# Kernel tuning notes

Measured on AMD Instinct MI355X. Metric: run time of the kernel, lower is better.

## Reference

```python
import jax, jax.numpy as jnp
import numpy as np

D_MODEL = 1024
N_HEADS = 16
D_K = D_MODEL // N_HEADS
D_HIDDEN = 2048
LN_EPS = 1e-5


def setup_inputs() -> dict:
    key = jax.random.key(0)
    ks = jax.random.split(key, 16)
    s = 0.02
    inp = {
        'x': jax.random.normal(ks[0], (4, 2048, D_MODEL), dtype=jnp.float32),
        'Wq': jax.random.normal(ks[1], (D_MODEL, D_MODEL), dtype=jnp.float32) * s,
        'bq': jnp.zeros((D_MODEL,), jnp.float32),
        'Wk': jax.random.normal(ks[2], (D_MODEL, D_MODEL), dtype=jnp.float32) * s,
        'bk': jnp.zeros((D_MODEL,), jnp.float32),
        'Wv': jax.random.normal(ks[3], (D_MODEL, D_MODEL), dtype=jnp.float32) * s,
        'bv': jnp.zeros((D_MODEL,), jnp.float32),
        'Wo': jax.random.normal(ks[4], (D_MODEL, D_MODEL), dtype=jnp.float32) * s,
        'bo': jnp.zeros((D_MODEL,), jnp.float32),
        'ln1_g': jnp.ones((D_MODEL,), jnp.float32),
        'ln1_b': jnp.zeros((D_MODEL,), jnp.float32),
        'ln2_g': jnp.ones((D_MODEL,), jnp.float32),
        'ln2_b': jnp.zeros((D_MODEL,), jnp.float32),
        'W1': jax.random.normal(ks[5], (2 * D_HIDDEN, D_MODEL), dtype=jnp.float32) * s,
        'b1': jnp.zeros((2 * D_HIDDEN,), jnp.float32),
        'W2': jax.random.normal(ks[6], (D_MODEL, D_HIDDEN), dtype=jnp.float32) * s,
        'b2': jnp.zeros((D_MODEL,), jnp.float32),
    }
    return inp


def _layernorm(x, g, b):
    mu = jnp.mean(x, axis=-1, keepdims=True)
    var = jnp.mean(jnp.square(x - mu), axis=-1, keepdims=True)
    return (x - mu) * jax.lax.rsqrt(var + LN_EPS) * g + b


def _attention(xn, Wq, bq, Wk, bk, Wv, bv, Wo, bo):
    B, S, _ = xn.shape
    def split_heads(t):  # [B,S,D] -> [B,H,S,Dk]
        return t.reshape(B, S, N_HEADS, D_K).transpose(0, 2, 1, 3)
    Q = split_heads(xn @ Wq.T + bq)
    K = split_heads(xn @ Wk.T + bk)
    V = split_heads(xn @ Wv.T + bv)
    scores = jnp.einsum('bhqd,bhkd->bhqk', Q, K) / jnp.float32(D_K ** 0.5)
    attn = jax.nn.softmax(scores, axis=-1)  # torch code does max-sub + softmax (same math)
    ctx = jnp.einsum('bhqk,bhkd->bhqd', attn, V)
    ctx = ctx.transpose(0, 2, 1, 3).reshape(B, S, D_MODEL)
    return ctx @ Wo.T + bo


def reference(x, Wq, bq, Wk, bk, Wv, bv, Wo, bo, ln1_g, ln1_b, ln2_g, ln2_b, W1, b1, W2, b2):
    # pre-norm attention block
    xn = _layernorm(x, ln1_g, ln1_b)
    x = x + _attention(xn, Wq, bq, Wk, bk, Wv, bv, Wo, bo)
    # pre-norm ReGLU FFN
    xn = _layernorm(x, ln2_g, ln2_b)
    h = xn @ W1.T + b1
    a, b_ = jnp.split(h, 2, axis=-1)
    h = jax.nn.relu(a) * b_
    x = x + (h @ W2.T + b2)
    return x
```

## Files before the change

kernel.cpp:

```cpp
#include <hip/hip_runtime.h>
#include <hip/hip_bf16.h>

typedef __attribute__((ext_vector_type(8))) short short8;
typedef __attribute__((ext_vector_type(4))) float floatx4;

#define LN_EPS 1e-5f
#define EXP2_SCALE 0.18033688011112042f

__device__ __forceinline__ float b2f(unsigned short u) {
    union { float f; unsigned int i; } x; x.i = ((unsigned int)u) << 16; return x.f;
}
__device__ __forceinline__ unsigned short f2b(float f) {
    union { float f; unsigned int i; } x; x.f = f;
    unsigned int r = x.i + 0x7fffu + ((x.i >> 16) & 1u);
    return (unsigned short)(r >> 16);
}
__device__ __forceinline__ float to_f(unsigned short u) { return b2f(u); }
__device__ __forceinline__ float to_f(float f) { return f; }
__device__ __forceinline__ unsigned int cvtpk(float a, float b) {
    unsigned int r;
    asm("v_cvt_pk_bf16_f32 %0, %1, %2" : "=v"(r) : "v"(a), "v"(b));
    return r;
}

__device__ __forceinline__ void async16(const unsigned short* g, unsigned short* l) {
    __builtin_amdgcn_global_load_lds(
        (const __attribute__((address_space(1))) unsigned int*)g,
        (__attribute__((address_space(3))) unsigned int*)l, 16, 0, 0);
}

template<typename T>
__device__ __forceinline__ void ln_row(const T* __restrict__ xr, const float* __restrict__ g,
                                       const float* __restrict__ bb, unsigned short* __restrict__ outr,
                                       float* red)
{
    const int tid = threadIdx.x;
    float v[4];
#pragma unroll
    for (int i = 0; i < 4; i++) v[i] = to_f(xr[tid + i * 256]);
    float s  = v[0] + v[1] + v[2] + v[3];
    float sq = v[0]*v[0] + v[1]*v[1] + v[2]*v[2] + v[3]*v[3];
#pragma unroll
    for (int o = 32; o >= 1; o >>= 1) {
        s  += __shfl_xor(s,  o, 64);
        sq += __shfl_xor(sq, o, 64);
    }
    const int wave = tid >> 6, lane = tid & 63;
    if (lane == 0) { red[wave] = s; red[4 + wave] = sq; }
    __syncthreads();
    s  = red[0] + red[1] + red[2] + red[3];
    sq = red[4] + red[5] + red[6] + red[7];
    const float mu  = s * (1.0f / 1024.0f);
    const float var = sq * (1.0f / 1024.0f) - mu * mu;
    const float rs  = rsqrtf(var + LN_EPS);
#pragma unroll
    for (int i = 0; i < 4; i++) {
        int c = tid + i * 256;
        outr[c] = f2b((v[i] - mu) * rs * g[c] + bb[c]);
    }
}

__global__ __launch_bounds__(256)
void prep_kernel(const float* __restrict__ Wq, const float* __restrict__ Wk,
                 const float* __restrict__ Wv, const float* __restrict__ Wo,
                 const float* __restrict__ W1, const float* __restrict__ W2,
                 unsigned short* __restrict__ wdst,
                 const float* __restrict__ x, const float* __restrict__ ln1g,
                 const float* __restrict__ ln1b, unsigned short* __restrict__ xn)
{
    __shared__ float red[8];
    if (blockIdx.x < 5120) {
        const size_t i = (size_t)(blockIdx.x * 256 + threadIdx.x) * 8;
        const float* src; size_t off;
        if (i < 4194304) {
            int w = (int)(i >> 20);
            src = (w == 0) ? Wq : (w == 1) ? Wk : (w == 2) ? Wv : Wo;
            off = i & 1048575;
        } else if (i < 8388608) { src = W1; off = i - 4194304; }
        else                    { src = W2; off = i - 8388608; }
        float4 a = *reinterpret_cast<const float4*>(src + off);
        float4 b = *reinterpret_cast<const float4*>(src + off + 4);
        short8 r;
        r[0] = (short)f2b(a.x); r[1] = (short)f2b(a.y);
        r[2] = (short)f2b(a.z); r[3] = (short)f2b(a.w);
        r[4] = (short)f2b(b.x); r[5] = (short)f2b(b.y);
        r[6] = (short)f2b(b.z); r[7] = (short)f2b(b.w);
        *reinterpret_cast<short8*>(wdst + i) = r;
    } else {
        const int row = blockIdx.x - 5120;
        ln_row<float>(x + (size_t)row * 1024, ln1g, ln1b, xn + (size_t)row * 1024, red);
    }
}

__global__ __launch_bounds__(256)
void ln_kernel(const unsigned short* __restrict__ x, const float* __restrict__ g,
               const float* __restrict__ bb, unsigned short* __restrict__ out)
{
    __shared__ float red[8];
    const int row = blockIdx.x;
    ln_row<unsigned short>(x + (size_t)row * 1024, g, bb, out + (size_t)row * 1024, red);
}

template<int EPI>
__global__ __launch_bounds__(256, 3)
void gemm_nt(const unsigned short* __restrict__ A, const unsigned short* __restrict__ B,
             const float* __restrict__ bias, const void* __restrict__ res,
             void* __restrict__ C, int M, int N, int K)
{
    __shared__ unsigned short As[128 * 64];
    __shared__ unsigned short Bs[128 * 64];
    const int m0 = blockIdx.y * 128, n0 = blockIdx.x * 128;
    const int tid = threadIdx.x, wave = tid >> 6, lane = tid & 63;
    const int wm = (wave >> 1) * 64, wn = (wave & 1) * 64;
    const int lrow = lane & 15, quad = lane >> 4;
    const int srow = wave * 32 + (lane >> 3);
    const int scol = (((lane & 7) ^ ((lane >> 3) & 7)) << 3);
    const int ca0 = (quad ^ (lrow & 7)) << 3;
    const int ca1 = ((quad + 4) ^ (lrow & 7)) << 3;

    floatx4 acc[4][4] = {};
    const unsigned short* gA = A + (size_t)(m0 + srow) * K + scol;
    const unsigned short* gB = B + (size_t)(n0 + srow) * K + scol;
    unsigned short* lA = &As[(wave * 32) * 64];
    unsigned short* lB = &Bs[(wave * 32) * 64];

    for (int k0 = 0; k0 < K; k0 += 64) {
        __syncthreads();
#pragma unroll
        for (int r = 0; r < 4; r++) {
            async16(gA + k0 + (size_t)(r * 8) * K, lA + r * 8 * 64);
            async16(gB + k0 + (size_t)(r * 8) * K, lB + r * 8 * 64);
        }
        __syncthreads();
#pragma unroll
        for (int ks = 0; ks < 2; ks++) {
            const int ca = ks ? ca1 : ca0;
            short8 af[4], bf[4];
#pragma unroll
            for (int i = 0; i < 4; i++)
                af[i] = *reinterpret_cast<const short8*>(&As[(wm + i * 16 + lrow) * 64 + ca]);
#pragma unroll
            for (int j = 0; j < 4; j++)
                bf[j] = *reinterpret_cast<const short8*>(&Bs[(wn + j * 16 + lrow) * 64 + ca]);
#pragma unroll
            for (int i = 0; i < 4; i++)
#pragma unroll
                for (int j = 0; j < 4; j++)
                    acc[i][j] = __builtin_amdgcn_mfma_f32_16x16x32_bf16(af[i], bf[j], acc[i][j], 0, 0, 0);
        }
    }

#pragma unroll
    for (int i = 0; i < 4; i++) {
        int rb = m0 + wm + i * 16 + quad * 4;
#pragma unroll
        for (int j = 0; j < 4; j++) {
            int col = n0 + wn + j * 16 + lrow;
            float bv = bias[col];
#pragma unroll
            for (int r = 0; r < 4; r++) {
                size_t idx = (size_t)(rb + r) * N + col;
                float v = acc[i][j][r] + bv;
                if (EPI == 1) {
                    v += ((const float*)res)[idx];
                    ((unsigned short*)C)[idx] = f2b(v);
                } else {
                    v += b2f(((const unsigned short*)res)[idx]);
                    ((float*)C)[idx] = v;
                }
            }
        }
    }
}

__global__ __launch_bounds__(256, 3)
void gemm_qkv(const unsigned short* __restrict__ A, const unsigned short* __restrict__ Wqkv,
              const float* __restrict__ bq, const float* __restrict__ bk, const float* __restrict__ bv,
              unsigned short* __restrict__ QK, unsigned short* __restrict__ Vt)
{
    __shared__ unsigned short As[128 * 64];
    __shared__ unsigned short Bs[128 * 64];
    const int part = blockIdx.x >> 3;
    const int m0 = blockIdx.y * 128, n0 = (blockIdx.x & 7) * 128;
    const int tid = threadIdx.x, wave = tid >> 6, lane = tid & 63;
    const int wm = (wave >> 1) * 64, wn = (wave & 1) * 64;
    const int lrow = lane & 15, quad = lane >> 4;
    const int srow = wave * 32 + (lane >> 3);
    const int scol = (((lane & 7) ^ ((lane >> 3) & 7)) << 3);
    const int ca0 = (quad ^ (lrow & 7)) << 3;
    const int ca1 = ((quad + 4) ^ (lrow & 7)) << 3;
    const unsigned short* B = Wqkv + (size_t)part * 1048576;
    const float* bias = (part == 0) ? bq : (part == 1) ? bk : bv;

    floatx4 acc[4][4] = {};
    const unsigned short* gA = A + (size_t)(m0 + srow) * 1024 + scol;
    const unsigned short* gB = B + (size_t)(n0 + srow) * 1024 + scol;
    unsigned short* lA = &As[(wave * 32) * 64];
    unsigned short* lB = &Bs[(wave * 32) * 64];

    for (int k0 = 0; k0 < 1024; k0 += 64) {
        __syncthreads();
#pragma unroll
        for (int r = 0; r < 4; r++) {
            async16(gA + k0 + (size_t)(r * 8) * 1024, lA + r * 8 * 64);
            async16(gB + k0 + (size_t)(r * 8) * 1024, lB + r * 8 * 64);
        }
        __syncthreads();
#pragma unroll
        for (int ks = 0; ks < 2; ks++) {
            const int ca = ks ? ca1 : ca0;
            short8 af[4], bf[4];
#pragma unroll
            for (int i = 0; i < 4; i++)
                af[i] = *reinterpret_cast<const short8*>(&As[(wm + i * 16 + lrow) * 64 + ca]);
#pragma unroll
            for (int j = 0; j < 4; j++)
                bf[j] = *reinterpret_cast<const short8*>(&Bs[(wn + j * 16 + lrow) * 64 + ca]);
#pragma unroll
            for (int i = 0; i < 4; i++)
#pragma unroll
                for (int j = 0; j < 4; j++)
                    acc[i][j] = __builtin_amdgcn_mfma_f32_16x16x32_bf16(af[i], bf[j], acc[i][j], 0, 0, 0);
        }
    }

#pragma unroll
    for (int i = 0; i < 4; i++) {
        int rb = m0 + wm + i * 16 + quad * 4;
#pragma unroll
        for (int j = 0; j < 4; j++) {
            int col = n0 + wn + j * 16 + lrow;
            float bv2 = bias[col];
            if (part == 0) {
#pragma unroll
                for (int r = 0; r < 4; r++)
                    QK[(size_t)(rb + r) * 1024 + col] = f2b((acc[i][j][r] + bv2) * EXP2_SCALE);
            } else if (part == 1) {
                unsigned short* dst = QK + 8388608;
#pragma unroll
                for (int r = 0; r < 4; r++)
                    dst[(size_t)(rb + r) * 1024 + col] = f2b(acc[i][j][r] + bv2);
            } else {
                int b = rb >> 11, spos = rb & 2047;
                int h = col >> 6, d = col & 63;
                unsigned short* dst = Vt + (((size_t)(b * 16 + h) * 64 + d) << 11) + spos;
                unsigned int u01 = cvtpk(acc[i][j][0] + bv2, acc[i][j][1] + bv2);
                unsigned int u23 = cvtpk(acc[i][j][2] + bv2, acc[i][j][3] + bv2);
                *reinterpret_cast<uint2*>(dst) = make_uint2(u01, u23);
            }
        }
    }
}

__global__ __launch_bounds__(256, 2)
void gemm_w1_reglu(const unsigned short* __restrict__ A, const unsigned short* __restrict__ B,
                   const float* __restrict__ bias, unsigned short* __restrict__ G)
{
    __shared__ unsigned short As[128 * 64];
    __shared__ unsigned short B0s[128 * 64];
    __shared__ unsigned short B1s[128 * 64];
    const int m0 = blockIdx.y * 128, n0 = blockIdx.x * 128;
    const int tid = threadIdx.x, wave = tid >> 6, lane = tid & 63;
    const int wm = (wave >> 1) * 64, wn = (wave & 1) * 64;
    const int lrow = lane & 15, quad = lane >> 4;
    const int srow = wave * 32 + (lane >> 3);
    const int scol = (((lane & 7) ^ ((lane >> 3) & 7)) << 3);
    const int ca0 = (quad ^ (lrow & 7)) << 3;
    const int ca1 = ((quad + 4) ^ (lrow & 7)) << 3;

    floatx4 acca[4][4] = {};
    floatx4 accb[4][4] = {};
    const unsigned short* gA  = A + (size_t)(m0 + srow) * 1024 + scol;
    const unsigned short* gB0 = B + (size_t)(n0 + srow) * 1024 + scol;
    const unsigned short* gB1 = B + (size_t)(2048 + n0 + srow) * 1024 + scol;
    unsigned short* lA  = &As [(wave * 32) * 64];
    unsigned short* lB0 = &B0s[(wave * 32) * 64];
    unsigned short* lB1 = &B1s[(wave * 32) * 64];

    for (int k0 = 0; k0 < 1024; k0 += 64) {
        __syncthreads();
#pragma unroll
        for (int r = 0; r < 4; r++) {
            async16(gA  + k0 + (size_t)(r * 8) * 1024, lA  + r * 8 * 64);
            async16(gB0 + k0 + (size_t)(r * 8) * 1024, lB0 + r * 8 * 64);
            async16(gB1 + k0 + (size_t)(r * 8) * 1024, lB1 + r * 8 * 64);
        }
        __syncthreads();
#pragma unroll
        for (int ks = 0; ks < 2; ks++) {
            const int ca = ks ? ca1 : ca0;
            short8 af[4], b0[4], b1[4];
#pragma unroll
            for (int i = 0; i < 4; i++)
                af[i] = *reinterpret_cast<const short8*>(&As[(wm + i * 16 + lrow) * 64 + ca]);
#pragma unroll
            for (int j = 0; j < 4; j++) {
                b0[j] = *reinterpret_cast<const short8*>(&B0s[(wn + j * 16 + lrow) * 64 + ca]);
                b1[j] = *reinterpret_cast<const short8*>(&B1s[(wn + j * 16 + lrow) * 64 + ca]);
            }
#pragma unroll
            for (int i = 0; i < 4; i++)
#pragma unroll
                for (int j = 0; j < 4; j++) {
                    acca[i][j] = __builtin_amdgcn_mfma_f32_16x16x32_bf16(af[i], b0[j], acca[i][j], 0, 0, 0);
                    accb[i][j] = __builtin_amdgcn_mfma_f32_16x16x32_bf16(af[i], b1[j], accb[i][j], 0, 0, 0);
                }
        }
    }

#pragma unroll
    for (int i = 0; i < 4; i++) {
        int rb = m0 + wm + i * 16 + quad * 4;
#pragma unroll
        for (int j = 0; j < 4; j++) {
            int col = n0 + wn + j * 16 + lrow;
            float ba = bias[col], bb2 = bias[2048 + col];
#pragma unroll
            for (int r = 0; r < 4; r++) {
                float va = acca[i][j][r] + ba;
                float vb = accb[i][j][r] + bb2;
                G[(size_t)(rb + r) * 2048 + col] = f2b(fmaxf(va, 0.0f) * vb);
            }
        }
    }
}

__global__ __launch_bounds__(256, 4)
void attn_kernel(const unsigned short* __restrict__ Qm, const unsigned short* __restrict__ Km,
                 const unsigned short* __restrict__ Vt, unsigned short* __restrict__ ctx)
{
    __shared__ unsigned short Ks[64 * 64];
    __shared__ unsigned short Vs[64 * 64];
    __shared__ unsigned short Ps[4][32][72];

    const int tid = threadIdx.x, wave = tid >> 6, lane = tid & 63;
    const int lrow = lane & 15, quad = lane >> 4;
    const int id = blockIdx.x + (blockIdx.y << 4);
    const int qb = id >> 6;
    const int bh = ((id & 7) << 3) + ((id >> 3) & 7);
    const size_t base  = (size_t)(bh >> 4) * 2048 * 1024 + (size_t)(bh & 15) * 64;
    const size_t vbase = (size_t)bh * 131072;
    const int q0 = qb * 128 + wave * 32;
    const int g_sub = (lane >> 3);
    const int g_col = (((lane & 7) ^ (g_sub & 7)) << 3);
    const int ca0 = (quad ^ (lrow & 7)) << 3;
    const int ca1 = ((quad + 4) ^ (lrow & 7)) << 3;

    short8 qf[2][2];
#pragma unroll
    for (int m = 0; m < 2; m++) {
        const unsigned short* qp = Qm + base + (size_t)(q0 + m * 16 + lrow) * 1024 + quad * 8;
        qf[m][0] = *reinterpret_cast<const short8*>(qp);
        qf[m][1] = *reinterpret_cast<const short8*>(qp + 32);
    }

    floatx4 o[2][4] = {};
    float li[2] = {0.f, 0.f};
    const floatx4 fzero = {0.f, 0.f, 0.f, 0.f};

    for (int t = 0; t < 32; t++) {
        const int k0 = t * 64;
        __syncthreads();
#pragma unroll
        for (int r = 0; r < 2; r++) {
            int krow = wave * 16 + r * 8 + g_sub;
            async16(Km + base + (size_t)(k0 + krow) * 1024 + g_col, &Ks[(wave * 16 + r * 8) * 64]);
            async16(Vt + vbase + (size_t)krow * 2048 + k0 + g_col,  &Vs[(wave * 16 + r * 8) * 64]);
        }
        __syncthreads();

        short8 kf0[4], kf1[4];
#pragma unroll
        for (int j = 0; j < 4; j++) {
            kf0[j] = *reinterpret_cast<const short8*>(&Ks[(j * 16 + lrow) * 64 + ca0]);
            kf1[j] = *reinterpret_cast<const short8*>(&Ks[(j * 16 + lrow) * 64 + ca1]);
        }
        floatx4 s4t[2][4];
        __builtin_amdgcn_s_setprio(1);
#pragma unroll
        for (int m = 0; m < 2; m++)
#pragma unroll
            for (int j = 0; j < 4; j++) {
                s4t[m][j] = __builtin_amdgcn_mfma_f32_16x16x32_bf16(kf0[j], qf[m][0], fzero, 0, 0, 0);
                s4t[m][j] = __builtin_amdgcn_mfma_f32_16x16x32_bf16(kf1[j], qf[m][1], s4t[m][j], 0, 0, 0);
            }
        __builtin_amdgcn_s_setprio(0);

#pragma unroll
        for (int m = 0; m < 2; m++) {
            float acc = 0.f;
#pragma unroll
            for (int j = 0; j < 4; j++) {
                float p0 = __builtin_amdgcn_exp2f(s4t[m][j][0]);
                float p1 = __builtin_amdgcn_exp2f(s4t[m][j][1]);
                float p2 = __builtin_amdgcn_exp2f(s4t[m][j][2]);
                float p3 = __builtin_amdgcn_exp2f(s4t[m][j][3]);
                acc += (p0 + p1) + (p2 + p3);
                uint2 pk = make_uint2(cvtpk(p0, p1), cvtpk(p2, p3));
                *reinterpret_cast<uint2*>(&Ps[wave][m * 16 + lrow][j * 16 + quad * 4]) = pk;
            }
            li[m] += acc;
        }
        __asm__ volatile("s_waitcnt lgkmcnt(0)" ::: "memory");

        short8 pf[2][2];
#pragma unroll
        for (int m = 0; m < 2; m++) {
            pf[m][0] = *reinterpret_cast<const short8*>(&Ps[wave][m * 16 + lrow][quad * 8]);
            pf[m][1] = *reinterpret_cast<const short8*>(&Ps[wave][m * 16 + lrow][32 + quad * 8]);
        }
#pragma unroll
        for (int jj = 0; jj < 4; jj++) {
            short8 vf0 = *reinterpret_cast<const short8*>(&Vs[(jj * 16 + lrow) * 64 + ca0]);
            short8 vf1 = *reinterpret_cast<const short8*>(&Vs[(jj * 16 + lrow) * 64 + ca1]);
            __builtin_amdgcn_s_setprio(1);
#pragma unroll
            for (int m = 0; m < 2; m++) {
                o[m][jj] = __builtin_amdgcn_mfma_f32_16x16x32_bf16(pf[m][0], vf0, o[m][jj], 0, 0, 0);
                o[m][jj] = __builtin_amdgcn_mfma_f32_16x16x32_bf16(pf[m][1], vf1, o[m][jj], 0, 0, 0);
            }
            __builtin_amdgcn_s_setprio(0);
        }
    }

#pragma unroll
    for (int m = 0; m < 2; m++) {
        float l = li[m];
        l += __shfl_xor(l, 16, 64);
        l += __shfl_xor(l, 32, 64);
        float inv = 1.0f / l;
#pragma unroll
        for (int r = 0; r < 4; r++) {
            float invr = __shfl(inv, quad * 4 + r, 64);
            int srow = q0 + m * 16 + quad * 4 + r;
#pragma unroll
            for (int jj = 0; jj < 4; jj++)
                ctx[base + (size_t)srow * 1024 + jj * 16 + lrow] = f2b(o[m][jj][r] * invr);
        }
    }
}

extern "C" void kernel_launch(void* const* d_in, const int* in_sizes, int n_in,
                              void* d_out, int out_size, void* d_ws, size_t ws_size,
                              hipStream_t stream) {
    const float* x    = (const float*)d_in[0];
    const float* Wq   = (const float*)d_in[1];
    const float* bq   = (const float*)d_in[2];
    const float* Wk   = (const float*)d_in[3];
    const float* bk   = (const float*)d_in[4];
    const float* Wv   = (const float*)d_in[5];
    const float* bv   = (const float*)d_in[6];
    const float* Wo   = (const float*)d_in[7];
    const float* bo   = (const float*)d_in[8];
    const float* ln1g = (const float*)d_in[9];
    const float* ln1b = (const float*)d_in[10];
    const float* ln2g = (const float*)d_in[11];
    const float* ln2b = (const float*)d_in[12];
    const float* W1   = (const float*)d_in[13];
    const float* b1   = (const float*)d_in[14];
    const float* W2   = (const float*)d_in[15];
    const float* b2   = (const float*)d_in[16];
    float* out = (float*)d_out;

    char* ws = (char*)d_ws;
    unsigned short* wflat = (unsigned short*)ws;
    unsigned short* wqb = wflat;
    unsigned short* wob = wflat + 3145728;
    unsigned short* w1b = wflat + 4194304;
    unsigned short* w2b = wflat + 8388608;
    unsigned short* xn  = (unsigned short*)(ws + 20971520);
    unsigned short* Qm  = (unsigned short*)(ws + 37748736);
    unsigned short* x1b = (unsigned short*)(ws + 37748736);
    unsigned short* Vt  = (unsigned short*)(ws + 71303168);
    unsigned short* g   = (unsigned short*)(ws + 71303168);

    dim3 blk(256);
    prep_kernel<<<13312, blk, 0, stream>>>(Wq, Wk, Wv, Wo, W1, W2, wflat, x, ln1g, ln1b, xn);
    gemm_qkv<<<dim3(24, 64), blk, 0, stream>>>(xn, wqb, bq, bk, bv, Qm, Vt);
    attn_kernel<<<dim3(16, 64), blk, 0, stream>>>(Qm, Qm + 8388608, Vt, xn);
    gemm_nt<1><<<dim3(8, 64), blk, 0, stream>>>(xn, wob, bo, x, x1b, 8192, 1024, 1024);
    ln_kernel<<<8192, blk, 0, stream>>>(x1b, ln2g, ln2b, xn);
    gemm_w1_reglu<<<dim3(16, 64), blk, 0, stream>>>(xn, w1b, b1, g);
    gemm_nt<2><<<dim3(8, 64), blk, 0, stream>>>(g, w2b, b2, x1b, out, 8192, 1024, 2048);
}
```

Baseline: 432.9 us.

## Prefetch K/V tiles into registers to overlap global loads with attention compute

Replaces the per-iteration async global-to-LDS loads with a register-staged software pipeline. The next K/V tile is loaded into registers while the current tile is computed, then written to LDS after a barrier. The aim is to hide global memory latency behind MFMA work in the flash-attention loop. In exchange it uses more registers and adds explicit waitcnt and barrier sequencing, which may lower occupancy.

Measured after the change: 446.7 us. +3.2%, slower.

```diff
diff --git a/kernel.cpp b/kernel.cpp
--- a/kernel.cpp
+++ b/kernel.cpp
@@ -358,17 +358,26 @@
     float li[2] = {0.f, 0.f};
     const floatx4 fzero = {0.f, 0.f, 0.f, 0.f};
 
-    for (int t = 0; t < 32; t++) {
-        const int k0 = t * 64;
-        __syncthreads();
-#pragma unroll
-        for (int r = 0; r < 2; r++) {
-            int krow = wave * 16 + r * 8 + g_sub;
-            async16(Km + base + (size_t)(k0 + krow) * 1024 + g_col, &Ks[(wave * 16 + r * 8) * 64]);
-            async16(Vt + vbase + (size_t)krow * 2048 + k0 + g_col,  &Vs[(wave * 16 + r * 8) * 64]);
-        }
-        __syncthreads();
-
+    const unsigned short* gK = Km + base  + (size_t)(wave * 16 + g_sub) * 1024 + g_col;
+    const unsigned short* gV = Vt + vbase + (size_t)(wave * 16 + g_sub) * 2048 + g_col;
+    unsigned short* lK = &Ks[(wave * 16) * 64] + lane * 8;
+    unsigned short* lV = &Vs[(wave * 16) * 64] + lane * 8;
+
+    uint4 kr0, kr1, vr0, vr1;
+    auto load_regs = [&](int k0) {
+        kr0 = *reinterpret_cast<const uint4*>(gK + (size_t)k0 * 1024);
+        kr1 = *reinterpret_cast<const uint4*>(gK + (size_t)k0 * 1024 + 8 * 1024);
+        vr0 = *reinterpret_cast<const uint4*>(gV + k0);
+        vr1 = *reinterpret_cast<const uint4*>(gV + k0 + 8 * 2048);
+    };
+    auto write_lds = [&]() {
+        *reinterpret_cast<uint4*>(lK)           = kr0;
+        *reinterpret_cast<uint4*>(lK + 8 * 64)  = kr1;
+        *reinterpret_cast<uint4*>(lV)           = vr0;
+        *reinterpret_cast<uint4*>(lV + 8 * 64)  = vr1;
+    };
+
+    auto compute = [&](int t) {
         short8 kf0[4], kf1[4];
 #pragma unroll
         for (int j = 0; j < 4; j++) {
@@ -420,6 +429,31 @@
                 o[m][jj] = __builtin_amdgcn_mfma_f32_16x16x32_bf16(pf[m][1], vf1, o[m][jj], 0, 0, 0);
             }
             __builtin_amdgcn_s_setprio(0);
+        }
+    };
+
+    load_regs(0);
+    __asm__ volatile("s_waitcnt vmcnt(0)" ::: "memory");
+    __builtin_amdgcn_sched_barrier(0);
+    write_lds();
+    load_regs(64);
+    __asm__ volatile("s_waitcnt lgkmcnt(0)" ::: "memory");
+    __builtin_amdgcn_s_barrier();
+    __builtin_amdgcn_sched_barrier(0);
+
+    for (int t = 0; t < 32; t++) {
+        compute(t);
+        if (t < 31) {
+            __builtin_amdgcn_sched_barrier(0);
+            __asm__ volatile("s_waitcnt vmcnt(0)" ::: "memory");
+            __builtin_amdgcn_s_barrier();
+            __builtin_amdgcn_sched_barrier(0);
+            write_lds();
+            if (t < 30) load_regs((t + 2) * 64);
+            __asm__ volatile("s_waitcnt lgkmcnt(0)" ::: "memory");
+            __builtin_amdgcn_sched_barrier(0);
+            __builtin_amdgcn_s_barrier();
+            __builtin_amdgcn_sched_barrier(0);
         }
     }
 
```

## Replace QKV and W1-ReGLU GEMMs with double-buffered 256x256 tile kernel

Applied to the files above, without the earlier changes.

Adds a templated 512-thread GEMM with 256x256 output tiles, double-buffered LDS, and loads of the next K-slice interleaved with MFMA work under raised wave priority. It replaces both the QKV projection and the W1 ReGLU GEMM. For ReGLU, the W1 rows are interleaved during weight prep so gate and value columns sit next to each other, and they are paired with a lane shuffle in the epilogue. The larger tile raises arithmetic intensity and hides load latency, at the cost of 128KB of LDS per block, lower occupancy, and extra barriers.

Result: slower. 513.9 us (+18.7%).

```diff
diff --git a/kernel.cpp b/kernel.cpp
--- a/kernel.cpp
+++ b/kernel.cpp
@@ -71,12 +71,17 @@
     __shared__ float red[8];
     if (blockIdx.x < 5120) {
         const size_t i = (size_t)(blockIdx.x * 256 + threadIdx.x) * 8;
-        const float* src; size_t off;
+        const float* src; size_t off; size_t dsti = i;
         if (i < 4194304) {
             int w = (int)(i >> 20);
             src = (w == 0) ? Wq : (w == 1) ? Wk : (w == 2) ? Wv : Wo;
             off = i & 1048575;
-        } else if (i < 8388608) { src = W1; off = i - 4194304; }
+        } else if (i < 8388608) {
+            src = W1; off = i - 4194304;
+            const size_t row = off >> 10, col = off & 1023;
+            const size_t nrow = (row < 2048) ? (row << 1) : (((row - 2048) << 1) | 1);
+            dsti = 4194304 + (nrow << 10) + col;
+        }
         else                    { src = W2; off = i - 8388608; }
         float4 a = *reinterpret_cast<const float4*>(src + off);
         float4 b = *reinterpret_cast<const float4*>(src + off + 4);
@@ -85,7 +90,7 @@
         r[2] = (short)f2b(a.z); r[3] = (short)f2b(a.w);
         r[4] = (short)f2b(b.x); r[5] = (short)f2b(b.y);
         r[6] = (short)f2b(b.z); r[7] = (short)f2b(b.w);
-        *reinterpret_cast<short8*>(wdst + i) = r;
+        *reinterpret_cast<short8*>(wdst + dsti) = r;
     } else {
         const int row = blockIdx.x - 5120;
         ln_row<float>(x + (size_t)row * 1024, ln1g, ln1b, xn + (size_t)row * 1024, red);
@@ -173,153 +178,159 @@
     }
 }
 
-__global__ __launch_bounds__(256, 3)
-void gemm_qkv(const unsigned short* __restrict__ A, const unsigned short* __restrict__ Wqkv,
-              const float* __restrict__ bq, const float* __restrict__ bk, const float* __restrict__ bv,
-              unsigned short* __restrict__ QK, unsigned short* __restrict__ Vt)
-{
-    __shared__ unsigned short As[128 * 64];
-    __shared__ unsigned short Bs[128 * 64];
-    const int part = blockIdx.x >> 3;
-    const int m0 = blockIdx.y * 128, n0 = (blockIdx.x & 7) * 128;
+template<int EPI>
+__global__ __launch_bounds__(512, 2)
+void gemm256(const unsigned short* __restrict__ A, const unsigned short* __restrict__ Bw,
+             const float* __restrict__ bq, const float* __restrict__ bk, const float* __restrict__ bv,
+             unsigned short* __restrict__ out0, unsigned short* __restrict__ out1)
+{
+    __shared__ unsigned short Asl[2][256 * 64];
+    __shared__ unsigned short Bsl[2][256 * 64];
     const int tid = threadIdx.x, wave = tid >> 6, lane = tid & 63;
-    const int wm = (wave >> 1) * 64, wn = (wave & 1) * 64;
     const int lrow = lane & 15, quad = lane >> 4;
-    const int srow = wave * 32 + (lane >> 3);
-    const int scol = (((lane & 7) ^ ((lane >> 3) & 7)) << 3);
-    const int ca0 = (quad ^ (lrow & 7)) << 3;
-    const int ca1 = ((quad + 4) ^ (lrow & 7)) << 3;
-    const unsigned short* B = Wqkv + (size_t)part * 1048576;
-    const float* bias = (part == 0) ? bq : (part == 1) ? bk : bv;
-
-    floatx4 acc[4][4] = {};
-    const unsigned short* gA = A + (size_t)(m0 + srow) * 1024 + scol;
-    const unsigned short* gB = B + (size_t)(n0 + srow) * 1024 + scol;
-    unsigned short* lA = &As[(wave * 32) * 64];
-    unsigned short* lB = &Bs[(wave * 32) * 64];
-
-    for (int k0 = 0; k0 < 1024; k0 += 64) {
-        __syncthreads();
-#pragma unroll
-        for (int r = 0; r < 4; r++) {
-            async16(gA + k0 + (size_t)(r * 8) * 1024, lA + r * 8 * 64);
-            async16(gB + k0 + (size_t)(r * 8) * 1024, lB + r * 8 * 64);
-        }
-        __syncthreads();
-#pragma unroll
-        for (int ks = 0; ks < 2; ks++) {
-            const int ca = ks ? ca1 : ca0;
-            short8 af[4], bf[4];
-#pragma unroll
-            for (int i = 0; i < 4; i++)
-                af[i] = *reinterpret_cast<const short8*>(&As[(wm + i * 16 + lrow) * 64 + ca]);
-#pragma unroll
-            for (int j = 0; j < 4; j++)
-                bf[j] = *reinterpret_cast<const short8*>(&Bs[(wn + j * 16 + lrow) * 64 + ca]);
-#pragma unroll
-            for (int i = 0; i < 4; i++)
-#pragma unroll
-                for (int j = 0; j < 4; j++)
-                    acc[i][j] = __builtin_amdgcn_mfma_f32_16x16x32_bf16(af[i], bf[j], acc[i][j], 0, 0, 0);
-        }
-    }
-
-#pragma unroll
-    for (int i = 0; i < 4; i++) {
-        int rb = m0 + wm + i * 16 + quad * 4;
-#pragma unroll
-        for (int j = 0; j < 4; j++) {
-            int col = n0 + wn + j * 16 + lrow;
-            float bv2 = bias[col];
-            if (part == 0) {
-#pragma unroll
-                for (int r = 0; r < 4; r++)
-                    QK[(size_t)(rb + r) * 1024 + col] = f2b((acc[i][j][r] + bv2) * EXP2_SCALE);
-            } else if (part == 1) {
-                unsigned short* dst = QK + 8388608;
-#pragma unroll
-                for (int r = 0; r < 4; r++)
-                    dst[(size_t)(rb + r) * 1024 + col] = f2b(acc[i][j][r] + bv2);
-            } else {
-                int b = rb >> 11, spos = rb & 2047;
-                int h = col >> 6, d = col & 63;
-                unsigned short* dst = Vt + (((size_t)(b * 16 + h) * 64 + d) << 11) + spos;
-                unsigned int u01 = cvtpk(acc[i][j][0] + bv2, acc[i][j][1] + bv2);
-                unsigned int u23 = cvtpk(acc[i][j][2] + bv2, acc[i][j][3] + bv2);
-                *reinterpret_cast<uint2*>(dst) = make_uint2(u01, u23);
-            }
-        }
-    }
-}
-
-__global__ __launch_bounds__(256, 2)
-void gemm_w1_reglu(const unsigned short* __restrict__ A, const unsigned short* __restrict__ B,
-                   const float* __restrict__ bias, unsigned short* __restrict__ G)
-{
-    __shared__ unsigned short As[128 * 64];
-    __shared__ unsigned short B0s[128 * 64];
-    __shared__ unsigned short B1s[128 * 64];
-    const int m0 = blockIdx.y * 128, n0 = blockIdx.x * 128;
-    const int tid = threadIdx.x, wave = tid >> 6, lane = tid & 63;
-    const int wm = (wave >> 1) * 64, wn = (wave & 1) * 64;
-    const int lrow = lane & 15, quad = lane >> 4;
-    const int srow = wave * 32 + (lane >> 3);
-    const int scol = (((lane & 7) ^ ((lane >> 3) & 7)) << 3);
-    const int ca0 = (quad ^ (lrow & 7)) << 3;
-    const int ca1 = ((quad + 4) ^ (lrow & 7)) << 3;
-
-    floatx4 acca[4][4] = {};
-    floatx4 accb[4][4] = {};
-    const unsigned short* gA  = A + (size_t)(m0 + srow) * 1024 + scol;
-    const unsigned short* gB0 = B + (size_t)(n0 + srow) * 1024 + scol;
-    const unsigned short* gB1 = B + (size_t)(2048 + n0 + srow) * 1024 + scol;
-    unsigned short* lA  = &As [(wave * 32) * 64];
-    unsigned short* lB0 = &B0s[(wave * 32) * 64];
-    unsigned short* lB1 = &B1s[(wave * 32) * 64];
-
-    for (int k0 = 0; k0 < 1024; k0 += 64) {
-        __syncthreads();
-#pragma unroll
-        for (int r = 0; r < 4; r++) {
-            async16(gA  + k0 + (size_t)(r * 8) * 1024, lA  + r * 8 * 64);
-            async16(gB0 + k0 + (size_t)(r * 8) * 1024, lB0 + r * 8 * 64);
-            async16(gB1 + k0 + (size_t)(r * 8) * 1024, lB1 + r * 8 * 64);
-        }
-        __syncthreads();
-#pragma unroll
-        for (int ks = 0; ks < 2; ks++) {
-            const int ca = ks ? ca1 : ca0;
-            short8 af[4], b0[4], b1[4];
-#pragma unroll
-            for (int i = 0; i < 4; i++)
-                af[i] = *reinterpret_cast<const short8*>(&As[(wm + i * 16 + lrow) * 64 + ca]);
-#pragma unroll
-            for (int j = 0; j < 4; j++) {
-                b0[j] = *reinterpret_cast<const short8*>(&B0s[(wn + j * 16 + lrow) * 64 + ca]);
-                b1[j] = *reinterpret_cast<const short8*>(&B1s[(wn + j * 16 + lrow) * 64 + ca]);
-            }
-#pragma unroll
-            for (int i = 0; i < 4; i++)
-#pragma unroll
-                for (int j = 0; j < 4; j++) {
-                    acca[i][j] = __builtin_amdgcn_mfma_f32_16x16x32_bf16(af[i], b0[j], acca[i][j], 0, 0, 0);
-                    accb[i][j] = __builtin_amdgcn_mfma_f32_16x16x32_bf16(af[i], b1[j], accb[i][j], 0, 0, 0);
+    const int wm = (wave >> 2) * 128, wn = (wave & 3) * 64;
+    const int m0 = blockIdx.y * 256;
+    int part, n0;
+    const unsigned short* B;
+    const float* bias;
+    if (EPI == 0) {
+        part = blockIdx.x >> 2; n0 = (blockIdx.x & 3) * 256;
+        B = Bw + (size_t)part * 1048576 + (size_t)n0 * 1024;
+        bias = (part == 0) ? bq : (part == 1) ? bk : bv;
+    } else {
+        part = 0; n0 = blockIdx.x * 256;
+        B = Bw + (size_t)n0 * 1024;
+        bias = bq;
+    }
+
+    const int ssub = lane >> 3;
+    const int schk = ((lane & 7) ^ ssub) << 3;
+    const unsigned short* gAs = A + (size_t)(m0 + wave * 8 + ssub) * 1024 + schk;
+    const unsigned short* gBs = B + (size_t)(wave * 8 + ssub) * 1024 + schk;
+
+    floatx4 acc[8][4] = {};
+
+    auto stA = [&](int slot, int rowbase, int kk) {
+        async16(gAs + (size_t)rowbase * 1024 + kk, &Asl[slot][rowbase * 64 + wave * 512]);
+    };
+    auto stB = [&](int slot, int rowbase, int kk) {
+        async16(gBs + (size_t)rowbase * 1024 + kk, &Bsl[slot][rowbase * 64 + wave * 512]);
+    };
+
+    stA(0, 0, 0); stA(0, 64, 0); stA(0, 128, 0); stA(0, 192, 0);
+    stB(0, 0, 0); stB(0, 64, 0); stB(0, 128, 0); stB(0, 192, 0);
+    __asm__ volatile("s_waitcnt vmcnt(0)" ::: "memory");
+    __builtin_amdgcn_s_barrier();
+
+    for (int t = 0; t < 16; t++) {
+        const int sl = t & 1, ns = sl ^ 1;
+        const int kk = (t + 1) << 6;
+        const bool more = (t < 15);
+#pragma unroll
+        for (int q = 0; q < 4; q++) {
+            if (more) {
+                if (q == 0)      { stA(ns, 0,   kk); stA(ns, 64,  kk); }
+                else if (q == 1) { stA(ns, 128, kk); stA(ns, 192, kk); }
+                else if (q == 2) { stB(ns, 0,   kk); stB(ns, 64,  kk); }
+                else             { stB(ns, 128, kk); stB(ns, 192, kk); }
+            }
+            const int mi0 = (q & 1) * 4, nj0 = (q >> 1) * 2;
+            short8 af[4][2], bf[2][2];
+#pragma unroll
+            for (int f = 0; f < 4; f++) {
+                const int row = wm + (mi0 + f) * 16 + lrow;
+#pragma unroll
+                for (int ks = 0; ks < 2; ks++)
+                    af[f][ks] = *reinterpret_cast<const short8*>(
+                        &Asl[sl][row * 64 + (((ks * 4 + quad) ^ (lrow & 7)) << 3)]);
+            }
+#pragma unroll
+            for (int f = 0; f < 2; f++) {
+                const int row = wn + (nj0 + f) * 16 + lrow;
+#pragma unroll
+                for (int ks = 0; ks < 2; ks++)
+                    bf[f][ks] = *reinterpret_cast<const short8*>(
+                        &Bsl[sl][row * 64 + (((ks * 4 + quad) ^ (lrow & 7)) << 3)]);
+            }
+            __builtin_amdgcn_s_barrier();
+            __builtin_amdgcn_s_setprio(1);
+#pragma unroll
+            for (int fi = 0; fi < 4; fi++)
+#pragma unroll
+                for (int fj = 0; fj < 2; fj++)
+#pragma unroll
+                    for (int ks = 0; ks < 2; ks++)
+                        acc[mi0 + fi][nj0 + fj] = __builtin_amdgcn_mfma_f32_16x16x32_bf16(
+                            af[fi][ks], bf[fj][ks], acc[mi0 + fi][nj0 + fj], 0, 0, 0);
+            __builtin_amdgcn_s_setprio(0);
+            __builtin_amdgcn_s_barrier();
+        }
+        if (more) {
+            __asm__ volatile("s_waitcnt vmcnt(0)" ::: "memory");
+            __builtin_amdgcn_s_barrier();
+        }
+    }
+
+    if (EPI == 0) {
+        if (part == 0) {
+#pragma unroll
+            for (int fi = 0; fi < 8; fi++) {
+                const int rb = m0 + wm + fi * 16 + quad * 4;
+#pragma unroll
+                for (int fj = 0; fj < 4; fj++) {
+                    const int col = n0 + wn + fj * 16 + lrow;
+                    const float bv2 = bias[col];
+#pragma unroll
+                    for (int r = 0; r < 4; r++)
+                        out0[(size_t)(rb + r) * 1024 + col] = f2b((acc[fi][fj][r] + bv2) * EXP2_SCALE);
                 }
-        }
-    }
-
-#pragma unroll
-    for (int i = 0; i < 4; i++) {
-        int rb = m0 + wm + i * 16 + quad * 4;
-#pragma unroll
-        for (int j = 0; j < 4; j++) {
-            int col = n0 + wn + j * 16 + lrow;
-            float ba = bias[col], bb2 = bias[2048 + col];
-#pragma unroll
-            for (int r = 0; r < 4; r++) {
-                float va = acca[i][j][r] + ba;
-                float vb = accb[i][j][r] + bb2;
-                G[(size_t)(rb + r) * 2048 + col] = f2b(fmaxf(va, 0.0f) * vb);
+            }
+        } else if (part == 1) {
+            unsigned short* dst = out0 + 8388608;
+#pragma unroll
+            for (int fi = 0; fi < 8; fi++) {
+                const int rb = m0 + wm + fi * 16 + quad * 4;
+#pragma unroll
+                for (int fj = 0; fj < 4; fj++) {
+                    const int col = n0 + wn + fj * 16 + lrow;
+                    const float bv2 = bias[col];
+#pragma unroll
+                    for (int r = 0; r < 4; r++)
+                        dst[(size_t)(rb + r) * 1024 + col] = f2b(acc[fi][fj][r] + bv2);
+                }
+            }
+        } else {
+#pragma unroll
+            for (int fi = 0; fi < 8; fi++) {
+                const int rb = m0 + wm + fi * 16 + quad * 4;
+                const int b = rb >> 11, spos = rb & 2047;
+#pragma unroll
+                for (int fj = 0; fj < 4; fj++) {
+                    const int col = n0 + wn + fj * 16 + lrow;
+                    const float bv2 = bias[col];
+                    const int h = col >> 6, d = col & 63;
+                    unsigned short* dst = out1 + (((size_t)(b * 16 + h) * 64 + d) << 11) + spos;
+                    unsigned int u01 = cvtpk(acc[fi][fj][0] + bv2, acc[fi][fj][1] + bv2);
+                    unsigned int u23 = cvtpk(acc[fi][fj][2] + bv2, acc[fi][fj][3] + bv2);
+                    *reinterpret_cast<uint2*>(dst) = make_uint2(u01, u23);
+                }
+            }
+        }
+    } else {
+#pragma unroll
+        for (int fi = 0; fi < 8; fi++) {
+            const int rb = m0 + wm + fi * 16 + quad * 4;
+#pragma unroll
+            for (int fj = 0; fj < 4; fj++) {
+                const int br = n0 + wn + fj * 16 + lrow;
+                const float bv2 = bias[((br & 1) << 11) + (br >> 1)];
+#pragma unroll
+                for (int r = 0; r < 4; r++) {
+                    float v = acc[fi][fj][r] + bv2;
+                    float w = __shfl_xor(v, 1, 64);
+                    if (!(lane & 1))
+                        out0[(size_t)(rb + r) * 2048 + (br >> 1)] = f2b(fmaxf(v, 0.0f) * w);
+                }
             }
         }
     }
@@ -476,10 +487,10 @@
 
     dim3 blk(256);
     prep_kernel<<<13312, blk, 0, stream>>>(Wq, Wk, Wv, Wo, W1, W2, wflat, x, ln1g, ln1b, xn);
-    gemm_qkv<<<dim3(24, 64), blk, 0, stream>>>(xn, wqb, bq, bk, bv, Qm, Vt);
+    gemm256<0><<<dim3(12, 32), dim3(512), 0, stream>>>(xn, wqb, bq, bk, bv, Qm, Vt);
     attn_kernel<<<dim3(16, 64), blk, 0, stream>>>(Qm, Qm + 8388608, Vt, xn);
     gemm_nt<1><<<dim3(8, 64), blk, 0, stream>>>(xn, wob, bo, x, x1b, 8192, 1024, 1024);
     ln_kernel<<<8192, blk, 0, stream>>>(x1b, ln2g, ln2b, xn);
-    gemm_w1_reglu<<<dim3(16, 64), blk, 0, stream>>>(xn, w1b, b1, g);
+    gemm256<1><<<dim3(16, 32), dim3(512), 0, stream>>>(xn, w1b, b1, nullptr, nullptr, g, nullptr);
     gemm_nt<2><<<dim3(8, 64), blk, 0, stream>>>(g, w2b, b2, x1b, out, 8192, 1024, 2048);
 }
```
